# Optimization experiments

Hardware: AMD Instinct MI355X
Metric: run time of the kernel (lower is better)

## Reference

```python
import jax, jax.numpy as jnp
import numpy as np

B, TQ, TV, H = 8, 2048, 2048, 1024
LN_EPS = 1e-5


def setup_inputs() -> dict:
    key = jax.random.key(0)
    k1, k2, k3, k4 = jax.random.split(key, 4)
    query = jax.random.normal(k1, (B, TQ, H), dtype=jnp.float32)
    value = jax.random.normal(k2, (B, TV, H), dtype=jnp.float32)
    # nn.Linear(2H -> H): weight [H, 2H], bias [H]
    bound = 1.0 / np.sqrt(2 * H)
    W = jax.random.uniform(k3, (H, 2 * H), minval=-bound, maxval=bound, dtype=jnp.float32)
    b = jax.random.uniform(k4, (H,), minval=-bound, maxval=bound, dtype=jnp.float32)
    gamma = jnp.ones((H,), dtype=jnp.float32)
    beta = jnp.zeros((H,), dtype=jnp.float32)
    return {"query": query, "value": value, "W": W, "b": b, "gamma": gamma, "beta": beta}


def reference(query, value, W, b, gamma, beta):
    # scores: [B, Tq, Tv]
    score = jnp.einsum("bqh,bvh->bqv", query, value)
    attn = jax.nn.softmax(score, axis=-1)
    context = jnp.einsum("bqv,bvh->bqh", attn, value)  # [B, Tq, H]
    combined = jnp.concatenate((context, query), axis=2)  # [B, Tq, 2H]
    proj = jnp.einsum("bqk,hk->bqh", combined, W) + b  # [B, Tq, H]
    mean = jnp.mean(proj, axis=-1, keepdims=True)
    var = jnp.mean(jnp.square(proj - mean), axis=-1, keepdims=True)
    out = (proj - mean) * jax.lax.rsqrt(var + LN_EPS) * gamma + beta
    return out
```

## Files before the change

### kernel.cpp

```cpp
#include <hip/hip_runtime.h>

typedef unsigned short u16;
typedef _Float16 f16;
typedef __attribute__((ext_vector_type(8))) _Float16 f16x8;
typedef __attribute__((ext_vector_type(4))) float f32x4;

#define B_  8
#define TQ_ 2048
#define TV_ 2048
#define H_  1024

__device__ __forceinline__ u16 f2h(float x) {
    union { f16 h; u16 u; } c; c.h = (f16)x; return c.u;
}
__device__ __forceinline__ float h2f(u16 u) {
    union { u16 u; f16 h; } c; c.u = u; return (float)c.h;
}

__device__ __forceinline__ void gload_lds16(const u16* g, u16* l) {
    typedef __attribute__((address_space(1))) const unsigned short GAS;
    typedef __attribute__((address_space(3))) unsigned short LAS;
    __builtin_amdgcn_global_load_lds((GAS*)g, (LAS*)l, 16, 0, 0);
}

__global__ __launch_bounds__(256) void k_cvt(const float4* __restrict__ x,
                                             ushort4* __restrict__ o) {
    long long i = (long long)blockIdx.x * 256 + threadIdx.x;
    float4 v = x[i];
    ushort4 h;
    h.x = f2h(v.x); h.y = f2h(v.y); h.z = f2h(v.z); h.w = f2h(v.w);
    o[i] = h;
}

#define SBAR() __builtin_amdgcn_sched_barrier(0)

template<int NH, int OM, int LDA, int LDB, int KK>
__global__ __launch_bounds__(512, 2) void k_gemm8(const u16* __restrict__ Ap,
                                                  const u16* __restrict__ Bp,
                                                  long long sA, long long sB,
                                                  int mnTiles, int gn,
                                                  void* __restrict__ Cv, long long sC,
                                                  int ldc, const float* __restrict__ bias,
                                                  const u16* __restrict__ qadd) {
    constexpr int BUFU = 16384 + NH * 8192;
    constexpr int NT = KK / 64;
    __shared__ __align__(16) u16 lds[2 * BUFU];

    const int nper = gridDim.x >> 3;
    const int g = (blockIdx.x & 7) * nper + (blockIdx.x >> 3);
    const int z = g / mnTiles;
    const int rem = g - z * mnTiles;
    const int bm = (rem / gn) * 256;
    const int bn = (rem % gn) * (NH * 128);

    const int tid = threadIdx.x;
    const int lane = tid & 63, wid = tid >> 6;
    const int wm = wid >> 2, wn = wid & 3;
    const int l16 = lane & 15, kg = lane >> 4;

    f32x4 acc[8][NH * 2];
    f32x4 zv = {0.f, 0.f, 0.f, 0.f};
#pragma unroll
    for (int i = 0; i < 8; ++i)
#pragma unroll
        for (int j = 0; j < NH * 2; ++j) acc[i][j] = zv;

    const u16* Ab = Ap + (long long)z * sA;
    const u16* Bb = Bp + (long long)z * sB;

    const int jst = (tid & 7) ^ ((tid >> 3) & 7);
    const int rst = tid >> 3;

    auto stageA = [&](int k0, int h, int obase) {
#pragma unroll
        for (int c = 0; c < 2; ++c) {
            int r = h * 128 + c * 64 + rst;
            gload_lds16(Ab + (long long)(bm + r) * LDA + k0 + jst * 8,
                        &lds[obase + h * 8192 + c * 4096 + tid * 8]);
        }
    };
    auto stageB = [&](int k0, int h, int rbase) {
#pragma unroll
        for (int c = 0; c < 2; ++c) {
            int r = h * 128 + c * 64 + rst;
            gload_lds16(Bb + (long long)(bn + r) * LDB + k0 + jst * 8,
                        &lds[rbase + h * 8192 + c * 4096 + tid * 8]);
        }
    };
    auto rdA = [&](int base, int mh, f16x8* dst) {
#pragma unroll
        for (int i = 0; i < 4; ++i) {
            int r = wm * 128 + mh * 64 + i * 16 + l16;
#pragma unroll
            for (int ks = 0; ks < 2; ++ks) {
                int js = (ks * 4 + kg) ^ (r & 7);
                dst[i * 2 + ks] = *(const f16x8*)&lds[base + r * 64 + js * 8];
            }
        }
    };
    auto rdB = [&](int base, int nh, f16x8* dst) {
#pragma unroll
        for (int jn = 0; jn < 2; ++jn) {
            int r = wn * (NH * 32) + nh * 32 + jn * 16 + l16;
#pragma unroll
            for (int ks = 0; ks < 2; ++ks) {
                int js = (ks * 4 + kg) ^ (r & 7);
                dst[jn * 2 + ks] = *(const f16x8*)&lds[base + r * 64 + js * 8];
            }
        }
    };

    stageA(0, 0, 0);
    stageA(0, 1, 0);
#pragma unroll
    for (int h = 0; h < NH; ++h) stageB(0, h, 16384);
    if (NT > 1) {
#pragma unroll
        for (int h = 0; h < NH; ++h) stageB(64, h, BUFU + 16384);
        if constexpr (NH == 2) asm volatile("s_waitcnt vmcnt(4)" ::: "memory");
        else                   asm volatile("s_waitcnt vmcnt(2)" ::: "memory");
    } else {
        asm volatile("s_waitcnt vmcnt(0)" ::: "memory");
    }
    __builtin_amdgcn_s_barrier();
    SBAR();

    f16x8 a0[8], a1[8], b0[4], b1[4];
#pragma unroll 1
    for (int t = 0; t < NT; ++t) {
        const int cur = t & 1;
        const int AB = cur * BUFU;
        const int BB = AB + 16384;
        const int OA = (cur ^ 1) * BUFU;
        const bool sa = (t + 1) < NT;
        const bool sb = (t + 2) < NT;
        if constexpr (NH == 2) {
            rdA(AB, 0, a0);
            rdB(BB, 0, b0);
            rdB(BB, 1, b1);
            if (sa) {
                stageA((t + 1) * 64, 0, OA);
                stageA((t + 1) * 64, 1, OA);
            }
            SBAR();
            __builtin_amdgcn_s_setprio(1);
#pragma unroll
            for (int i = 0; i < 4; ++i)
#pragma unroll
                for (int jn = 0; jn < 2; ++jn)
#pragma unroll
                    for (int ks = 0; ks < 2; ++ks)
                        acc[i][jn] = __builtin_amdgcn_mfma_f32_16x16x32_f16(a0[i * 2 + ks], b0[jn * 2 + ks], acc[i][jn], 0, 0, 0);
#pragma unroll
            for (int i = 0; i < 4; ++i)
#pragma unroll
                for (int jn = 0; jn < 2; ++jn)
#pragma unroll
                    for (int ks = 0; ks < 2; ++ks)
                        acc[i][2 + jn] = __builtin_amdgcn_mfma_f32_16x16x32_f16(a0[i * 2 + ks], b1[jn * 2 + ks], acc[i][2 + jn], 0, 0, 0);
            __builtin_amdgcn_s_setprio(0);
            __builtin_amdgcn_s_barrier();
            SBAR();
            rdA(AB, 1, a1);
            if (sb) {
                stageB((t + 2) * 64, 0, BB);
                stageB((t + 2) * 64, 1, BB);
            }
            SBAR();
            __builtin_amdgcn_s_setprio(1);
#pragma unroll
            for (int i = 0; i < 4; ++i)
#pragma unroll
                for (int jn = 0; jn < 2; ++jn)
#pragma unroll
                    for (int ks = 0; ks < 2; ++ks)
                        acc[4 + i][2 + jn] = __builtin_amdgcn_mfma_f32_16x16x32_f16(a1[i * 2 + ks], b1[jn * 2 + ks], acc[4 + i][2 + jn], 0, 0, 0);
#pragma unroll
            for (int i = 0; i < 4; ++i)
#pragma unroll
                for (int jn = 0; jn < 2; ++jn)
#pragma unroll
                    for (int ks = 0; ks < 2; ++ks)
                        acc[4 + i][jn] = __builtin_amdgcn_mfma_f32_16x16x32_f16(a1[i * 2 + ks], b0[jn * 2 + ks], acc[4 + i][jn], 0, 0, 0);
            __builtin_amdgcn_s_setprio(0);
            if (sb)      asm volatile("s_waitcnt vmcnt(4)" ::: "memory");
            else if (sa) asm volatile("s_waitcnt vmcnt(0)" ::: "memory");
            __builtin_amdgcn_s_barrier();
            SBAR();
        } else {
            rdA(AB, 0, a0);
            rdB(BB, 0, b0);
            rdA(AB, 1, a1);
            if (sa) {
                stageA((t + 1) * 64, 0, OA);
                stageA((t + 1) * 64, 1, OA);
            }
            SBAR();
            __builtin_amdgcn_s_setprio(1);
#pragma unroll
            for (int i = 0; i < 4; ++i)
#pragma unroll
                for (int jn = 0; jn < 2; ++jn)
#pragma unroll
                    for (int ks = 0; ks < 2; ++ks)
                        acc[i][jn] = __builtin_amdgcn_mfma_f32_16x16x32_f16(a0[i * 2 + ks], b0[jn * 2 + ks], acc[i][jn], 0, 0, 0);
            __builtin_amdgcn_s_setprio(0);
            __builtin_amdgcn_s_barrier();
            SBAR();
            if (sb) stageB((t + 2) * 64, 0, BB);
            SBAR();
            __builtin_amdgcn_s_setprio(1);
#pragma unroll
            for (int i = 0; i < 4; ++i)
#pragma unroll
                for (int jn = 0; jn < 2; ++jn)
#pragma unroll
                    for (int ks = 0; ks < 2; ++ks)
                        acc[4 + i][jn] = __builtin_amdgcn_mfma_f32_16x16x32_f16(a1[i * 2 + ks], b0[jn * 2 + ks], acc[4 + i][jn], 0, 0, 0);
            __builtin_amdgcn_s_setprio(0);
            if (sb)      asm volatile("s_waitcnt vmcnt(2)" ::: "memory");
            else if (sa) asm volatile("s_waitcnt vmcnt(0)" ::: "memory");
            __builtin_amdgcn_s_barrier();
            SBAR();
        }
    }

    const int colBase = bn + wn * (NH * 32);
    const int rowBase = bm + wm * 128;
#pragma unroll
    for (int mi = 0; mi < 8; ++mi) {
#pragma unroll
        for (int nj = 0; nj < NH * 2; ++nj) {
            int col = colBase + nj * 16 + l16;
            float badd = (OM != 1 && bias) ? bias[col] : 0.f;
#pragma unroll
            for (int r = 0; r < 4; ++r) {
                long long row = rowBase + mi * 16 + kg * 4 + r;
                long long idx = (long long)z * sC + row * (long long)ldc + col;
                float vv = acc[mi][nj][r] + badd;
                if constexpr (OM == 1) {
                    ((u16*)Cv)[idx] = f2h(vv);
                } else if constexpr (OM == 2) {
                    ((float*)Cv)[idx] = vv + h2f(qadd[idx]);
                } else {
                    ((float*)Cv)[idx] = vv;
                }
            }
        }
    }
}

__global__ __launch_bounds__(256) void k_softmax(float* __restrict__ S) {
    float* row = S + (long long)blockIdx.x * TV_;
    u16* prow = (u16*)row;
    int t = threadIdx.x;
    float4 a = *(const float4*)(row + t * 4);
    float4 c = *(const float4*)(row + 1024 + t * 4);
    float m = fmaxf(fmaxf(fmaxf(a.x, a.y), fmaxf(a.z, a.w)),
                    fmaxf(fmaxf(c.x, c.y), fmaxf(c.z, c.w)));
#pragma unroll
    for (int o = 32; o; o >>= 1) m = fmaxf(m, __shfl_xor(m, o));
    __shared__ float rm[4], rs[4];
    if ((t & 63) == 0) rm[t >> 6] = m;
    __syncthreads();
    m = fmaxf(fmaxf(rm[0], rm[1]), fmaxf(rm[2], rm[3]));
    float e0 = __expf(a.x - m), e1 = __expf(a.y - m), e2 = __expf(a.z - m), e3 = __expf(a.w - m);
    float e4 = __expf(c.x - m), e5 = __expf(c.y - m), e6 = __expf(c.z - m), e7 = __expf(c.w - m);
    float s = ((e0 + e1) + (e2 + e3)) + ((e4 + e5) + (e6 + e7));
#pragma unroll
    for (int o = 32; o; o >>= 1) s += __shfl_xor(s, o);
    if ((t & 63) == 0) rs[t >> 6] = s;
    __syncthreads();
    s = rs[0] + rs[1] + rs[2] + rs[3];
    float inv = 1.f / s;
    ushort4 o0, o1;
    o0.x = f2h(e0 * inv); o0.y = f2h(e1 * inv); o0.z = f2h(e2 * inv); o0.w = f2h(e3 * inv);
    o1.x = f2h(e4 * inv); o1.y = f2h(e5 * inv); o1.z = f2h(e6 * inv); o1.w = f2h(e7 * inv);
    __syncthreads();
    *(ushort4*)(prow + t * 4) = o0;
    *(ushort4*)(prow + 1024 + t * 4) = o1;
}

__global__ __launch_bounds__(256) void k_layernorm(float* __restrict__ O,
                                                   const float* __restrict__ g,
                                                   const float* __restrict__ b) {
    float* row = O + (long long)blockIdx.x * H_;
    int t = threadIdx.x;
    float4 x = *(const float4*)(row + t * 4);
    float s1 = x.x + x.y + x.z + x.w;
    float s2 = x.x * x.x + x.y * x.y + x.z * x.z + x.w * x.w;
#pragma unroll
    for (int o = 32; o; o >>= 1) { s1 += __shfl_xor(s1, o); s2 += __shfl_xor(s2, o); }
    __shared__ float r1[4], r2[4];
    if ((t & 63) == 0) { r1[t >> 6] = s1; r2[t >> 6] = s2; }
    __syncthreads();
    s1 = r1[0] + r1[1] + r1[2] + r1[3];
    s2 = r2[0] + r2[1] + r2[2] + r2[3];
    float mean = s1 * (1.f / H_);
    float var = s2 * (1.f / H_) - mean * mean;
    float rstd = rsqrtf(fmaxf(var, 0.f) + 1e-5f);
    float4 gv = *(const float4*)(g + t * 4);
    float4 bv = *(const float4*)(b + t * 4);
    float4 o;
    o.x = (x.x - mean) * rstd * gv.x + bv.x;
    o.y = (x.y - mean) * rstd * gv.y + bv.y;
    o.z = (x.z - mean) * rstd * gv.z + bv.z;
    o.w = (x.w - mean) * rstd * gv.w + bv.w;
    *(float4*)(row + t * 4) = o;
}

extern "C" void kernel_launch(void* const* d_in, const int* in_sizes, int n_in,
                              void* d_out, int out_size, void* d_ws, size_t ws_size,
                              hipStream_t stream) {
    const float* q     = (const float*)d_in[0];
    const float* v     = (const float*)d_in[1];
    const float* W     = (const float*)d_in[2];
    const float* bias  = (const float*)d_in[3];
    const float* gamma = (const float*)d_in[4];
    const float* beta  = (const float*)d_in[5];
    float* out = (float*)d_out;
    char* ws = (char*)d_ws;

    const long long nQV = (long long)B_ * TQ_ * H_;
    const long long nW  = (long long)H_ * 2 * H_;

    u16* Qh  = (u16*)ws;
    u16* Vh  = Qh + nQV;
    u16* Wh  = Vh + nQV;
    u16* VWT = Wh + nW;
    u16* QW  = VWT + nQV;
    float* S = (float*)(QW + nQV);
    size_t fixedBytes = (size_t)((char*)S - ws);
    const size_t perZ = (size_t)TQ_ * TV_ * 4;

    int Zc = 1;
    for (int cand = 4; cand >= 1; cand >>= 1) {
        if (fixedBytes + (size_t)cand * perZ <= ws_size) { Zc = cand; break; }
    }

    k_cvt<<<dim3(nQV / 4 / 256), dim3(256), 0, stream>>>((const float4*)q, (ushort4*)Qh);
    k_cvt<<<dim3(nQV / 4 / 256), dim3(256), 0, stream>>>((const float4*)v, (ushort4*)Vh);
    k_cvt<<<dim3(nW / 4 / 256),  dim3(256), 0, stream>>>((const float4*)W, (ushort4*)Wh);

    k_gemm8<2, 1, 2048, 1024, 1024><<<dim3(256), dim3(512), 0, stream>>>(
        Wh, Vh, 0, (long long)TV_ * H_,
        32, 8, VWT, (long long)H_ * TV_, TV_, nullptr, nullptr);

    k_gemm8<2, 1, 1024, 2048, 1024><<<dim3(256), dim3(512), 0, stream>>>(
        Qh, Wh + H_, 0, 0,
        256, 4, QW, 0, H_, nullptr, nullptr);

    for (int c0 = 0; c0 < B_; c0 += Zc) {
        k_gemm8<2, 0, 1024, 1024, 1024><<<dim3(Zc * 64), dim3(512), 0, stream>>>(
            Qh + (long long)c0 * TQ_ * H_, Vh + (long long)c0 * TV_ * H_,
            (long long)TQ_ * H_, (long long)TV_ * H_,
            64, 8, S, (long long)TQ_ * TV_, TV_, nullptr, nullptr);
        k_softmax<<<dim3(Zc * TQ_), dim3(256), 0, stream>>>(S);
        k_gemm8<1, 2, 4096, 2048, 2048><<<dim3(Zc * 64), dim3(512), 0, stream>>>(
            (const u16*)S, VWT + (long long)c0 * H_ * TV_,
            (long long)TQ_ * 4096, (long long)H_ * TV_,
            64, 8, out + (long long)c0 * TQ_ * H_, (long long)TQ_ * H_, H_,
            bias, QW + (long long)c0 * TQ_ * H_);
    }

    k_layernorm<<<dim3(B_ * TQ_), dim3(256), 0, stream>>>(out, gamma, beta);
}
```

Measured before the change: 323.4 us.

## Restructure GEMM main loop into unrolled-by-two ping-pong phases with finer staging

Rewrites the k_gemm8 K-loop as two unrolled iterations per pass over fixed LDS buffers. Each pass is split into four (or two) compute phases, and each phase reads a slice of fragments from LDS, issues one stage of global->LDS loads, then runs 16 MFMAs behind a barrier plus an lgkmcnt wait. The aim is to spread global loads and LDS reads more evenly across the MFMA work and to drop the per-iteration buffer index arithmetic. In exchange it adds more barriers per K-step, which may cost synchronisation overhead, and it now requires an even tile count.

```diff
diff --git a/kernel.cpp b/kernel.cpp
--- a/kernel.cpp
+++ b/kernel.cpp
@@ -33,6 +33,12 @@
 }
 
 #define SBAR() __builtin_amdgcn_sched_barrier(0)
+#define VMCNT(n) asm volatile("s_waitcnt vmcnt(" #n ")" ::: "memory")
+#define PHASE_MID() do { SBAR(); __builtin_amdgcn_s_barrier(); \
+    asm volatile("s_waitcnt lgkmcnt(0)" ::: "memory"); SBAR(); \
+    __builtin_amdgcn_s_setprio(1); } while (0)
+#define PHASE_END() do { __builtin_amdgcn_s_setprio(0); SBAR(); \
+    __builtin_amdgcn_s_barrier(); SBAR(); } while (0)
 
 template<int NH, int OM, int LDA, int LDB, int KK>
 __global__ __launch_bounds__(512, 2) void k_gemm8(const u16* __restrict__ Ap,
@@ -44,6 +50,7 @@
                                                   const u16* __restrict__ qadd) {
     constexpr int BUFU = 16384 + NH * 8192;
     constexpr int NT = KK / 64;
+    static_assert(NT % 2 == 0, "NT must be even");
     __shared__ __align__(16) u16 lds[2 * BUFU];
 
     const int nper = gridDim.x >> 3;
@@ -109,119 +116,103 @@
             }
         }
     };
-
-    stageA(0, 0, 0);
-    stageA(0, 1, 0);
-#pragma unroll
-    for (int h = 0; h < NH; ++h) stageB(0, h, 16384);
-    if (NT > 1) {
-#pragma unroll
-        for (int h = 0; h < NH; ++h) stageB(64, h, BUFU + 16384);
-        if constexpr (NH == 2) asm volatile("s_waitcnt vmcnt(4)" ::: "memory");
-        else                   asm volatile("s_waitcnt vmcnt(2)" ::: "memory");
+    auto MF = [&](int ar, int ac, f16x8* A, f16x8* B) {
+#pragma unroll
+        for (int i = 0; i < 4; ++i)
+#pragma unroll
+            for (int jn = 0; jn < 2; ++jn)
+#pragma unroll
+                for (int ks = 0; ks < 2; ++ks)
+                    acc[ar + i][ac + jn] = __builtin_amdgcn_mfma_f32_16x16x32_f16(
+                        A[i * 2 + ks], B[jn * 2 + ks], acc[ar + i][ac + jn], 0, 0, 0);
+    };
+
+    constexpr int AB0 = 0, BB0 = 16384;
+    constexpr int AB1 = BUFU, BB1 = BUFU + 16384;
+
+    f16x8 a0[8], a1[8], b0[4], b1[4];
+
+    if constexpr (NH == 2) {
+        stageA(0, 0, AB0);
+        stageA(0, 1, AB0);
+        stageB(0, 0, BB0);
+        stageB(0, 1, BB0);
+        stageB(64, 1, BB1);
+        stageA(64, 0, AB1);
+        VMCNT(4);
+        __builtin_amdgcn_s_barrier();
+        SBAR();
+
+#pragma unroll 1
+        for (int t = 0; t < NT; t += 2) {
+            const bool sb = (t + 2) < NT;
+            rdA(AB0, 0, a0);
+            rdB(BB0, 0, b0);
+            stageA((t + 1) * 64, 1, AB1);
+            PHASE_MID(); MF(0, 0, a0, b0); PHASE_END();
+            rdB(BB0, 1, b1);
+            stageB((t + 1) * 64, 0, BB1);
+            PHASE_MID(); MF(0, 2, a0, b1); PHASE_END();
+            rdA(AB0, 1, a1);
+            if (sb) stageB((t + 2) * 64, 0, BB0);
+            PHASE_MID(); MF(4, 2, a1, b1); PHASE_END();
+            if (sb) stageA((t + 2) * 64, 0, AB0);
+            PHASE_MID(); MF(4, 0, a1, b0);
+            __builtin_amdgcn_s_setprio(0); SBAR();
+            if (sb) { VMCNT(4); } else { VMCNT(0); }
+            __builtin_amdgcn_s_barrier(); SBAR();
+            rdA(AB1, 0, a0);
+            rdB(BB1, 0, b0);
+            if (sb) stageA((t + 2) * 64, 1, AB0);
+            PHASE_MID(); MF(0, 0, a0, b0); PHASE_END();
+            rdB(BB1, 1, b1);
+            if (sb) stageB((t + 2) * 64, 1, BB0);
+            PHASE_MID(); MF(0, 2, a0, b1); PHASE_END();
+            rdA(AB1, 1, a1);
+            if (sb) stageB((t + 3) * 64, 1, BB1);
+            PHASE_MID(); MF(4, 2, a1, b1); PHASE_END();
+            if (sb) stageA((t + 3) * 64, 0, AB1);
+            PHASE_MID(); MF(4, 0, a1, b0);
+            __builtin_amdgcn_s_setprio(0); SBAR();
+            if (sb) { VMCNT(4); }
+            __builtin_amdgcn_s_barrier(); SBAR();
+        }
     } else {
-        asm volatile("s_waitcnt vmcnt(0)" ::: "memory");
-    }
-    __builtin_amdgcn_s_barrier();
-    SBAR();
-
-    f16x8 a0[8], a1[8], b0[4], b1[4];
+        stageA(0, 0, AB0);
+        stageA(0, 1, AB0);
+        stageB(0, 0, BB0);
+        stageB(64, 0, BB1);
+        VMCNT(2);
+        __builtin_amdgcn_s_barrier();
+        SBAR();
+
 #pragma unroll 1
-    for (int t = 0; t < NT; ++t) {
-        const int cur = t & 1;
-        const int AB = cur * BUFU;
-        const int BB = AB + 16384;
-        const int OA = (cur ^ 1) * BUFU;
-        const bool sa = (t + 1) < NT;
-        const bool sb = (t + 2) < NT;
-        if constexpr (NH == 2) {
-            rdA(AB, 0, a0);
-            rdB(BB, 0, b0);
-            rdB(BB, 1, b1);
-            if (sa) {
-                stageA((t + 1) * 64, 0, OA);
-                stageA((t + 1) * 64, 1, OA);
+        for (int t = 0; t < NT; t += 2) {
+            const bool sb = (t + 2) < NT;
+            rdA(AB0, 0, a0);
+            rdB(BB0, 0, b0);
+            stageA((t + 1) * 64, 0, AB1);
+            PHASE_MID(); MF(0, 0, a0, b0); PHASE_END();
+            rdA(AB0, 1, a1);
+            stageA((t + 1) * 64, 1, AB1);
+            if (sb) stageB((t + 2) * 64, 0, BB0);
+            PHASE_MID(); MF(4, 0, a1, b0);
+            __builtin_amdgcn_s_setprio(0); SBAR();
+            if (sb) { VMCNT(2); } else { VMCNT(0); }
+            __builtin_amdgcn_s_barrier(); SBAR();
+            rdA(AB1, 0, a0);
+            rdB(BB1, 0, b0);
+            if (sb) stageA((t + 2) * 64, 0, AB0);
+            PHASE_MID(); MF(0, 0, a0, b0); PHASE_END();
+            rdA(AB1, 1, a1);
+            if (sb) {
+                stageA((t + 2) * 64, 1, AB0);
+                stageB((t + 3) * 64, 0, BB1);
             }
-            SBAR();
-            __builtin_amdgcn_s_setprio(1);
-#pragma unroll
-            for (int i = 0; i < 4; ++i)
-#pragma unroll
-                for (int jn = 0; jn < 2; ++jn)
-#pragma unroll
-                    for (int ks = 0; ks < 2; ++ks)
-                        acc[i][jn] = __builtin_amdgcn_mfma_f32_16x16x32_f16(a0[i * 2 + ks], b0[jn * 2 + ks], acc[i][jn], 0, 0, 0);
-#pragma unroll
-            for (int i = 0; i < 4; ++i)
-#pragma unroll
-                for (int jn = 0; jn < 2; ++jn)
-#pragma unroll
-                    for (int ks = 0; ks < 2; ++ks)
-                        acc[i][2 + jn] = __builtin_amdgcn_mfma_f32_16x16x32_f16(a0[i * 2 + ks], b1[jn * 2 + ks], acc[i][2 + jn], 0, 0, 0);
-            __builtin_amdgcn_s_setprio(0);
-            __builtin_amdgcn_s_barrier();
-            SBAR();
-            rdA(AB, 1, a1);
-            if (sb) {
-                stageB((t + 2) * 64, 0, BB);
-                stageB((t + 2) * 64, 1, BB);
-            }
-            SBAR();
-            __builtin_amdgcn_s_setprio(1);
-#pragma unroll
-            for (int i = 0; i < 4; ++i)
-#pragma unroll
-                for (int jn = 0; jn < 2; ++jn)
-#pragma unroll
-                    for (int ks = 0; ks < 2; ++ks)
-                        acc[4 + i][2 + jn] = __builtin_amdgcn_mfma_f32_16x16x32_f16(a1[i * 2 + ks], b1[jn * 2 + ks], acc[4 + i][2 + jn], 0, 0, 0);
-#pragma unroll
-            for (int i = 0; i < 4; ++i)
-#pragma unroll
-                for (int jn = 0; jn < 2; ++jn)
-#pragma unroll
-                    for (int ks = 0; ks < 2; ++ks)
-                        acc[4 + i][jn] = __builtin_amdgcn_mfma_f32_16x16x32_f16(a1[i * 2 + ks], b0[jn * 2 + ks], acc[4 + i][jn], 0, 0, 0);
-            __builtin_amdgcn_s_setprio(0);
-            if (sb)      asm volatile("s_waitcnt vmcnt(4)" ::: "memory");
-            else if (sa) asm volatile("s_waitcnt vmcnt(0)" ::: "memory");
-            __builtin_amdgcn_s_barrier();
-            SBAR();
-        } else {
-            rdA(AB, 0, a0);
-            rdB(BB, 0, b0);
-            rdA(AB, 1, a1);
-            if (sa) {
-                stageA((t + 1) * 64, 0, OA);
-                stageA((t + 1) * 64, 1, OA);
-            }
-            SBAR();
-            __builtin_amdgcn_s_setprio(1);
-#pragma unroll
-            for (int i = 0; i < 4; ++i)
-#pragma unroll
-                for (int jn = 0; jn < 2; ++jn)
-#pragma unroll
-                    for (int ks = 0; ks < 2; ++ks)
-                        acc[i][jn] = __builtin_amdgcn_mfma_f32_16x16x32_f16(a0[i * 2 + ks], b0[jn * 2 + ks], acc[i][jn], 0, 0, 0);
-            __builtin_amdgcn_s_setprio(0);
-            __builtin_amdgcn_s_barrier();
-            SBAR();
-            if (sb) stageB((t + 2) * 64, 0, BB);
-            SBAR();
-            __builtin_amdgcn_s_setprio(1);
-#pragma unroll
-            for (int i = 0; i < 4; ++i)
-#pragma unroll
-                for (int jn = 0; jn < 2; ++jn)
-#pragma unroll
-                    for (int ks = 0; ks < 2; ++ks)
-                        acc[4 + i][jn] = __builtin_amdgcn_mfma_f32_16x16x32_f16(a1[i * 2 + ks], b0[jn * 2 + ks], acc[4 + i][jn], 0, 0, 0);
-            __builtin_amdgcn_s_setprio(0);
-            if (sb)      asm volatile("s_waitcnt vmcnt(2)" ::: "memory");
-            else if (sa) asm volatile("s_waitcnt vmcnt(0)" ::: "memory");
-            __builtin_amdgcn_s_barrier();
-            SBAR();
+            PHASE_MID(); MF(4, 0, a1, b0);
+            __builtin_amdgcn_s_setprio(0); SBAR();
+            if (sb) { VMCNT(2); }
+            __builtin_amdgcn_s_barrier(); SBAR();
         }
     }
 
```

New measurement: 336.7 us. +4.1%, slower.
